# Performance work log

Measured on AMD Instinct MI355X. Metric: run time of the kernel, lower is better.

## Reference

```python
import jax, jax.numpy as jnp
import numpy as np

_S = np.float32(1.0 / np.sqrt(2.0))
_lo = np.array([_S, _S], np.float32)   # dec_lo reversed == rec_lo for db1
_hi = np.array([_S, -_S], np.float32)  # dec_hi reversed == rec_hi for db1
# filters[k][i,j]: k=0 LL/2, k=1 hi(i)*lo(j), k=2 lo(i)*hi(j), k=3 hi*hi  (matches torch unsqueeze outer products)
DEC = np.stack([np.outer(_lo, _lo) / 2.0, np.outer(_hi, _lo), np.outer(_lo, _hi), np.outer(_hi, _hi)]).astype(np.float32)
INV = np.stack([np.outer(_lo, _lo) * 2.0, np.outer(_hi, _lo), np.outer(_lo, _hi), np.outer(_hi, _hi)]).astype(np.float32)
INV_FLIP = np.ascontiguousarray(INV[:, ::-1, ::-1])  # spatially flipped for conv_transpose-as-dilated-conv

DN = ('NCHW', 'OIHW', 'NCHW')


def wt(x):
    # single grouped (depthwise x4) strided conv == per-channel loop in the original
    N, C, H, W = x.shape
    k = jnp.broadcast_to(jnp.asarray(DEC)[None], (C, 4, 2, 2)).reshape(C * 4, 1, 2, 2)
    r = jax.lax.conv_general_dilated(x, k, (2, 2), 'VALID', dimension_numbers=DN, feature_group_count=C)
    r = r.reshape(N, C, 4, H // 2, W // 2)
    r = jnp.concatenate([r[:, :, :1], (r[:, :, 1:] + 1.0) / 2.0], axis=2)  # detail remap
    return r.reshape(N, 4 * C, H // 2, W // 2)


def iwt(v):
    N, C4, H, W = v.shape
    C = C4 // 4
    r = v.reshape(N, C, 4, H, W)
    r = jnp.concatenate([r[:, :, :1], 2.0 * r[:, :, 1:] - 1.0], axis=2).reshape(N, C4, H, W)
    k = jnp.broadcast_to(jnp.asarray(INV_FLIP)[None], (C, 4, 2, 2))
    # conv_transpose2d(stride=2, k=2) == dilated conv with lhs_dilation=2, pad 1, flipped kernel
    return jax.lax.conv_general_dilated(r, k, (1, 1), ((1, 1), (1, 1)), lhs_dilation=(2, 2),
                                        dimension_numbers=DN, feature_group_count=C)


def ws_conv(x, w, b, pad):
    # weight standardization: subtract mean over (in,kh,kw), divide by per-filter std (unbiased) + 1e-5
    wc = w - w.mean(axis=(1, 2, 3), keepdims=True)
    std = wc.reshape(w.shape[0], -1).std(axis=1, ddof=1).reshape(-1, 1, 1, 1) + 1e-5
    y = jax.lax.conv_general_dilated(x, wc / std, (1, 1), ((pad, pad), (pad, pad)), dimension_numbers=DN)
    return y if b is None else y + b[None, :, None, None]


def gn(x, g, b, G):
    N, C, H, W = x.shape
    xr = x.reshape(N, G, -1)
    m = xr.mean(-1, keepdims=True)
    v = xr.var(-1, keepdims=True)
    xr = (xr - m) * jax.lax.rsqrt(v + 1e-5)
    return xr.reshape(N, C, H, W) * g[None, :, None, None] + b[None, :, None, None]


def lrelu(t):
    return jnp.where(t > 0, t, 0.2 * t)


def setup_inputs() -> dict:
    key = jax.random.key(0)
    ks = iter(jax.random.split(key, 32))
    f32 = jnp.float32
    d = {}
    d['x'] = jax.random.normal(next(ks), (16, 3, 256, 256), f32)
    def wgt(shape):
        return 0.05 * jax.random.normal(next(ks), shape, f32)
    def bias(n):
        return 0.01 * jax.random.normal(next(ks), (n,), f32)
    c = 16
    d['conv1_w'], d['conv1_b'] = wgt((c, 12, 3, 3)), bias(c)
    d['conv2_w'], d['conv2_b'] = wgt((4 * c, 4 * c, 3, 3)), bias(4 * c)
    d['conv3_w'], d['conv3_b'] = wgt((16 * c, 16 * c, 3, 3)), bias(16 * c)
    d['conv4_w'], d['conv4_b'] = wgt((64 * c, 64 * c, 3, 3)), bias(64 * c)
    d['convd1_w'], d['convd1_b'] = wgt((12, c, 3, 3)), bias(12)
    d['convd2_w'], d['convd2_b'] = wgt((c, 2 * c, 3, 3)), bias(c)
    d['convd3_w'], d['convd3_b'] = wgt((4 * c, 8 * c, 3, 3)), bias(4 * c)
    d['convd4_w'], d['convd4_b'] = wgt((16 * c, 32 * c, 3, 3)), bias(16 * c)
    d['final_w'] = wgt((2, 3, 1, 1))
    for name, n in (('gn1', c), ('gn2', 4 * c), ('gn3', 16 * c), ('gn4', 64 * c)):
        d[name + '_w'] = 1.0 + 0.1 * jax.random.normal(next(ks), (n,), f32)
        d[name + '_b'] = 0.01 * jax.random.normal(next(ks), (n,), f32)
    return d


def reference(x, conv1_w, conv1_b, conv2_w, conv2_b, conv3_w, conv3_b, conv4_w, conv4_b,
              convd1_w, convd1_b, convd2_w, convd2_b, convd3_w, convd3_b, convd4_w, convd4_b,
              final_w, gn1_w, gn1_b, gn2_w, gn2_b, gn3_w, gn3_b, gn4_w, gn4_b):
    w1 = wt(x)
    c1 = gn(lrelu(ws_conv(w1, conv1_w, conv1_b, 1)), gn1_w, gn1_b, 2)
    w2 = wt(c1)
    c2 = gn(lrelu(ws_conv(w2, conv2_w, conv2_b, 1)), gn2_w, gn2_b, 8)
    w3 = wt(c2)
    c3 = gn(lrelu(ws_conv(w3, conv3_w, conv3_b, 1)), gn3_w, gn3_b, 32)
    w4 = wt(c3)
    c4 = gn(lrelu(ws_conv(w4, conv4_w, conv4_b, 1)), gn4_w, gn4_b, 128)
    c5 = gn(lrelu(ws_conv(c4, conv4_w, conv4_b, 1)), gn4_w, gn4_b, 128)
    c6 = ws_conv(c5, conv4_w, conv4_b, 1)
    ic4 = lrelu(c6 + w4)
    iw4 = jnp.concatenate([c3, iwt(ic4)], axis=1)
    ic3 = gn(lrelu(ws_conv(iw4, convd4_w, convd4_b, 1)), gn3_w, gn3_b, 32)
    iw3 = jnp.concatenate([c2, iwt(ic3)], axis=1)
    ic2 = gn(lrelu(ws_conv(iw3, convd3_w, convd3_b, 1)), gn2_w, gn2_b, 8)
    iw2 = jnp.concatenate([c1, iwt(ic2)], axis=1)
    ic1 = gn(lrelu(ws_conv(iw2, convd2_w, convd2_b, 1)), gn1_w, gn1_b, 2)
    iw1 = lrelu(ws_conv(ic1, convd1_w, convd1_b, 1))
    y = ws_conv(iwt(iw1), final_w, None, 0)
    return y
```

## Files before the change

### kernel.cpp

```cpp
#include <hip/hip_runtime.h>
#include <math.h>


#define NB 16

typedef _Float16 f16;
typedef _Float16 f16x8 __attribute__((ext_vector_type(8)));
typedef _Float16 f16x4 __attribute__((ext_vector_type(4)));
typedef float f32x4 __attribute__((ext_vector_type(4)));
typedef unsigned int u32;

#define LLDS16(gp, lp)                                                          \
  __builtin_amdgcn_global_load_lds((const __attribute__((address_space(1))) u32*)(const void*)(gp), \
                                   (__attribute__((address_space(3))) u32*)(void*)(lp), 16, 0, 0)

__device__ __forceinline__ void ws_reduce(const float* wp, int fan, float* red,
                                          float& mean, float& inv) {
  float s = 0.f, s2 = 0.f;
  for (int i = threadIdx.x; i < fan; i += 256) { float v = wp[i]; s += v; s2 += v * v; }
  red[threadIdx.x] = s; red[256 + threadIdx.x] = s2;
  __syncthreads();
  for (int st = 128; st > 0; st >>= 1) {
    if (threadIdx.x < st) {
      red[threadIdx.x] += red[threadIdx.x + st];
// ... 37 lines not shown
  const float* wp = w + (size_t)oi * fan;
  float mean, inv; ws_reduce(wp, fan, red, mean, inv);
  for (int i = threadIdx.x; i < fan; i += 256) {
    int ci = i / 9, tap = i - ci * 9;
    o[((size_t)tap * Cout + oi) * Cin + ci] = (f16)((wp[i] - mean) * inv);
  }
}

__device__ __forceinline__ void halo_write(f16* buf, int C, int H, int W, int t) {
  int c8s = C >> 3;
  int c8 = t % c8s; int q = t / c8s;
  int P = 2 * (W + 2) + 2 * H;
  int b = q % P; int n = q / P;
  int y, x;
  if (b < W + 2) { y = 0; x = b; }
  else if (b < 2 * (W + 2)) { y = H + 1; x = b - (W + 2); }
  else { int bb = b - 2 * (W + 2); y = 1 + (bb >> 1); x = (bb & 1) ? (W + 1) : 0; }
  size_t a = (((size_t)n * (H + 2) + y) * (W + 2) + x) * C + c8 * 8;
  *(f16x8*)(buf + a) = (f16x8){0, 0, 0, 0, 0, 0, 0, 0};
}

__global__ void halo2_kernel(f16* b0, int c0, int h0, int w0, int n0,
                             f16* b1, int c1, int h1, int w1, int total) {
  int idx = blockIdx.x * 256 + threadIdx.x;
  if (idx >= total) return;
  if (idx < n0) halo_write(b0, c0, h0, w0, idx);
  else halo_write(b1, c1, h1, w1, idx - n0);
}

__global__ void zero_halo_kernel(f16* __restrict__ buf, int C, int H, int W, int total8) {
  int idx = blockIdx.x * 256 + threadIdx.x;
  if (idx >= total8) return;
  halo_write(buf, C, H, W, idx);
}

__global__ void wt_kernel(const float* __restrict__ in, float* __restrict__ out,
                          int C, int Ho, int Wo, int total) {
  int idx = blockIdx.x * 256 + threadIdx.x;
  if (idx >= total) return;
  int w = idx % Wo; int t = idx / Wo;
  int h = t % Ho; t /= Ho;
  int c = t % C; int n = t / C;
  int Wi = 2 * Wo;
  const float* ip = in + (((size_t)n * C + c) * (2 * Ho) + 2 * h) * Wi + 2 * w;
  float a = ip[0], b = ip[1], cc = ip[Wi], d = ip[Wi + 1];
  size_t cs = (size_t)Ho * Wo;
  float* op = out + (((size_t)n * 4 * C + 4 * c) * Ho + h) * Wo + w;
  op[0]      = 0.25f * (a + b + cc + d);
  op[cs]     = 0.25f * (a + b - cc - d) + 0.5f;
  op[2 * cs] = 0.25f * (a - b + cc - d) + 0.5f;
  op[3 * cs] = 0.25f * (a - b - cc + d) + 0.5f;
}

__global__ void iwt_kernel(const float* __restrict__ v, float* __restrict__ out,
                           int C, int H, int W, int c_off, int Ctot, int total) {
  int idx = blockIdx.x * 256 + threadIdx.x;
  if (idx >= total) return;
  int w = idx % W; int t = idx / W;
  int h = t % H; t /= H;
  int c = t % C; int n = t / C;
  size_t cs = (size_t)H * W;
  const float* vp = v + (((size_t)n * 4 * C + 4 * c) * H + h) * W + w;
  float v0 = vp[0];
  float v1 = 2.f * vp[cs] - 1.f;
  float v2 = 2.f * vp[2 * cs] - 1.f;
  float v3 = 2.f * vp[3 * cs] - 1.f;
  int Wo = 2 * W;
  float* op = out + (((size_t)n * Ctot + c_off + c) * (2 * H) + 2 * h) * (size_t)Wo + 2 * w;
  op[0]      = v0 + 0.5f * ( v1 + v2 + v3);
  op[1]      = v0 + 0.5f * ( v1 - v2 - v3);
  op[Wo]     = v0 + 0.5f * (-v1 + v2 - v3);
  op[Wo + 1] = v0 + 0.5f * (-v1 - v2 + v3);
}

__global__ void copycat_kernel(const float* __restrict__ src, float* __restrict__ dst,
                               int C, int HW, int Ctot, int total) {
  int idx = blockIdx.x * 256 + threadIdx.x;
  if (idx >= total) return;
  int p = idx % HW; int t = idx / HW;
  int c = t % C; int n = t / C;
  dst[((size_t)n * Ctot + c) * HW + p] = src[idx];
}

__global__ __launch_bounds__(256) void to_nhwc_pad_kernel(const float* __restrict__ in,
                                                          f16* __restrict__ out,
                                                          int C, int H, int W) {
  __shared__ f16 sm[32][264];
  int HW = H * W;
  int p0 = blockIdx.x * 256, c0 = blockIdx.y * 32, n = blockIdx.z;
  int t = threadIdx.x;
  const float* ip = in + ((size_t)n * C + c0) * HW + p0;
#pragma unroll 8
  for (int r = 0; r < 32; ++r) sm[r][t] = (f16)ip[(size_t)r * HW + t];
  __syncthreads();
#pragma unroll
  for (int i = 0; i < 4; ++i) {
    int c = t + i * 256;
    int pl = c >> 2, cio = (c & 3) * 8;
    f16x8 v;
#pragma unroll
    for (int u = 0; u < 8; ++u) v[u] = sm[cio + u][pl];
    int p = p0 + pl; int y = p / W; int x = p - y * W;
    *(f16x8*)(out + (((size_t)n * (H + 2) + y + 1) * (W + 2) + x + 1) * C + c0 + cio) = v;
  }
}

__global__ __launch_bounds__(256) void gn_nhwc_kernel(
    const float* __restrict__ in, const float* __restrict__ stats,
    const float* __restrict__ gamma, const float* __restrict__ beta,
    f16* __restrict__ out, int C, int H, int W, int G) {
  __shared__ f16 sm[32][264];
  int HW = H * W;
  int p0 = blockIdx.x * 256, c0 = blockIdx.y * 32, n = blockIdx.z;
  int t = threadIdx.x;
  int cpg = C / G;
  const float* ip = in + ((size_t)n * C + c0) * HW + p0;
#pragma unroll 8
  for (int r = 0; r < 32; ++r) {
    int c = c0 + r; int g = c / cpg;
    float mean = stats[(n * G + g) * 2], inv = stats[(n * G + g) * 2 + 1];
    float ga = gamma[c], be = beta[c];
    sm[r][t] = (f16)((ip[(size_t)r * HW + t] - mean) * inv * ga + be);
  }
  __syncthreads();
#pragma unroll
  for (int i = 0; i < 4; ++i) {
    int c = t + i * 256;
    int pl = c >> 2, cio = (c & 3) * 8;
    f16x8 v;
#pragma unroll
    for (int u = 0; u < 8; ++u) v[u] = sm[cio + u][pl];
    int p = p0 + pl; int y = p / W; int x = p - y * W;
    *(f16x8*)(out + (((size_t)n * (H + 2) + y + 1) * (W + 2) + x + 1) * C + c0 + cio) = v;
  }
}

__global__ void iwt_final_kernel(const float* __restrict__ v, const float* __restrict__ w,
                                 float* __restrict__ out, int total) {
  int idx = blockIdx.x * 256 + threadIdx.x;
  if (idx >= total) return;
  int ww = idx % 128; int t = idx / 128;
  int hh = t % 128; int n = t / 128;
  size_t cs = (size_t)128 * 128;
  float y0[3], y1[3], y2[3], y3[3];
#pragma unroll
  for (int c = 0; c < 3; ++c) {
    const float* vp = v + ((size_t)n * 12 + 4 * c) * cs + (size_t)hh * 128 + ww;
    float v0 = vp[0];
    float v1 = 2.f * vp[cs] - 1.f, v2 = 2.f * vp[2 * cs] - 1.f, v3 = 2.f * vp[3 * cs] - 1.f;
    y0[c] = v0 + 0.5f * ( v1 + v2 + v3);
    y1[c] = v0 + 0.5f * ( v1 - v2 - v3);
    y2[c] = v0 + 0.5f * (-v1 + v2 - v3);
    y3[c] = v0 + 0.5f * (-v1 - v2 + v3);
  }
  float w0 = w[0], w1 = w[1], w2 = w[2], w3 = w[3], w4 = w[4], w5 = w[5];
  size_t ocs = (size_t)256 * 256;
  float* o0 = out + (size_t)n * 2 * ocs + (size_t)(2 * hh) * 256 + 2 * ww;
  o0[0]   = w0 * y0[0] + w1 * y0[1] + w2 * y0[2];
  o0[1]   = w0 * y1[0] + w1 * y1[1] + w2 * y1[2];
  o0[256] = w0 * y2[0] + w1 * y2[1] + w2 * y2[2];
  o0[257] = w0 * y3[0] + w1 * y3[1] + w2 * y3[2];
  float* o1 = o0 + ocs;
  o1[0]   = w3 * y0[0] + w4 * y0[1] + w5 * y0[2];
  o1[1]   = w3 * y1[0] + w4 * y1[1] + w5 * y1[2];
  o1[256] = w3 * y2[0] + w4 * y2[1] + w5 * y2[2];
  o1[257] = w3 * y3[0] + w4 * y3[1] + w5 * y3[2];
}

__global__ __launch_bounds__(256) void conv_mfma5_kernel(
    const f16* __restrict__ A, const f16* __restrict__ Wp,
    f16* __restrict__ part, int Cin, int H, int W, int Cout, int HW) {
  constexpr int BM = 128, BN = 128, BK = 64;
  __shared__ f16 Asm[BM * BK];
  __shared__ f16 Bsm[BN * BK];

  const int tid = threadIdx.x;
  const int w = tid >> 6, lane = tid & 63;
  const int m0 = blockIdx.x * BM;
  const int co0 = blockIdx.y * BN;
  const int Wp2 = W + 2;

  const f16* gA[4]; const f16* gB[4];
  int lOff[4];
#pragma unroll
  for (int e = 0; e < 4; ++e) {
    int c = e * 256 + tid;
    int r = c >> 3, j = c & 7;
    int jx = j ^ (r & 7);
    int m = m0 + r; int n = m / HW; int p = m - n * HW;
    int y = p / W; int x = p - y * W;
    gA[e] = A + (((size_t)n * (H + 2) + y + 1) * Wp2 + (x + 1)) * Cin + jx * 8;
    gB[e] = Wp + (size_t)(co0 + r) * Cin + jx * 8;
    lOff[e] = (e * 256 + w * 64) * 8;
  }

  const int wm = w & 1, wn = w >> 1;
  const int lr = lane & 15, quad = lane >> 4;
  int aoffs[4][2], boffs[4][2];
#pragma unroll
  for (int i = 0; i < 4; ++i)
#pragma unroll
    for (int kk = 0; kk < 2; ++kk) {
      int r = wm * 64 + i * 16 + lr;
      int cidx = kk * 4 + quad;
      aoffs[i][kk] = (r * 8 + (cidx ^ (r & 7))) * 8;
      int rb = wn * 64 + i * 16 + lr;
      boffs[i][kk] = (rb * 8 + (cidx ^ (rb & 7))) * 8;
    }

  f32x4 acc[4][4];
#pragma unroll
  for (int i = 0; i < 4; ++i)
#pragma unroll
    for (int j = 0; j < 4; ++j) acc[i][j] = (f32x4){0.f, 0.f, 0.f, 0.f};

  const int kpt = Cin >> 6;
  const int nit = (9 * kpt) / gridDim.z;
  const size_t bstride = (size_t)Cout * Cin;

  int it0 = blockIdx.z * nit;
  int tap = it0 / kpt, kc = (it0 - tap * kpt) << 6;

  for (int ii = 0; ii < nit; ++ii) {
    int dy = tap / 3 - 1, dx = tap % 3 - 1;
    long offA = ((long)dy * Wp2 + dx) * Cin + kc;
    long offB = (long)tap * bstride + kc;
    __syncthreads();
#pragma unroll
    for (int e = 0; e < 4; ++e) {
      LLDS16(gA[e] + offA, Asm + lOff[e]);
      LLDS16(gB[e] + offB, Bsm + lOff[e]);
    }
    __syncthreads();

    f16x8 af[4][2], bf[4][2];
#pragma unroll
    for (int i = 0; i < 4; ++i)
#pragma unroll
      for (int kk = 0; kk < 2; ++kk) {
        af[i][kk] = *(const f16x8*)&Asm[aoffs[i][kk]];
        bf[i][kk] = *(const f16x8*)&Bsm[boffs[i][kk]];
      }
#pragma unroll
    for (int kk = 0; kk < 2; ++kk)
#pragma unroll
      for (int i = 0; i < 4; ++i)
#pragma unroll
        for (int j = 0; j < 4; ++j)
          acc[i][j] = __builtin_amdgcn_mfma_f32_16x16x32_f16(af[i][kk], bf[j][kk], acc[i][j], 0, 0, 0);

    kc += 64;
    if (kc == Cin) { kc = 0; ++tap; }
  }

  const size_t pbase = (size_t)blockIdx.z * NB * Cout * HW;
#pragma unroll
  for (int i = 0; i < 4; ++i) {
    int mg = m0 + wm * 64 + i * 16 + quad * 4;
    int n = mg / HW, p = mg - n * HW;
#pragma unroll
    for (int j = 0; j < 4; ++j) {
      int co = co0 + wn * 64 + j * 16 + lr;
      f32x4 v = acc[i][j];
      f16x4 h;
#pragma unroll
      for (int r = 0; r < 4; ++r) h[r] = (f16)v[r];
      *(f16x4*)&part[pbase + ((size_t)n * Cout + co) * HW + p] = h;
    }
  }
}

__global__ __launch_bounds__(256) void reduceS_kernel(
    const f16* __restrict__ part, const float* __restrict__ bias,
    const float* __restrict__ add, float* __restrict__ out,
    int Cout, int HW, int S, int do_lrelu, int total4) {
  int idx = blockIdx.x * 256 + threadIdx.x;
  if (idx >= total4) return;
  size_t sstride = (size_t)NB * Cout * HW;
  int hw4 = HW >> 2;
  int p4 = idx % hw4; int t = idx / hw4;
  int c = t % Cout;
  size_t eoff = (size_t)t * HW + p4 * 4;
  float b = bias[c];
  f32x4 o = {b, b, b, b};
  for (int s = 0; s < S; ++s) {
    f16x4 a = *(const f16x4*)(part + s * sstride + eoff);
#pragma unroll
    for (int r = 0; r < 4; ++r) o[r] += (float)a[r];
  }
  if (add) {
    f32x4 av = *(const f32x4*)(add + eoff);
#pragma unroll
    for (int r = 0; r < 4; ++r) o[r] += av[r];
  }
  if (do_lrelu)
#pragma unroll
    for (int r = 0; r < 4; ++r) o[r] = o[r] > 0.f ? o[r] : 0.2f * o[r];
  *(f32x4*)(out + eoff) = o;
}

__global__ __launch_bounds__(256) void conv_mfma2_kernel(
    const f16* __restrict__ A, const f16* __restrict__ Wp,
    const float* __restrict__ bias, float* __restrict__ out,
    int Cin, int H, int W, int Cout, int HW, int do_lrelu) {
  constexpr int BM = 128, BN = 64, BK = 64;
  __shared__ f16 Asm[BM * BK];
  __shared__ f16 Bsm[BN * BK];

  const int tid = threadIdx.x;
  const int w = tid >> 6, lane = tid & 63;
  const int m0 = blockIdx.x * BM;
  const int co0 = blockIdx.y * BN;
  const int Wp2 = W + 2;

  const f16* gA[4];
  int lAoff[4];
#pragma unroll
  for (int e = 0; e < 4; ++e) {
    int c = e * 256 + tid;
    int r = c >> 3, j = c & 7;
    int jx = j ^ (r & 7);
    int m = m0 + r; int n = m / HW; int p = m - n * HW;
    int y = p / W; int x = p - y * W;
    gA[e] = A + (((size_t)n * (H + 2) + y + 1) * Wp2 + (x + 1)) * Cin + jx * 8;
    lAoff[e] = (e * 256 + w * 64) * 8;
  }
  const f16* gB[2];
  int lBoff[2];
#pragma unroll
  for (int e = 0; e < 2; ++e) {
    int c = e * 256 + tid;
    int r = c >> 3, j = c & 7;
    int jx = j ^ (r & 7);
    gB[e] = Wp + (size_t)(co0 + r) * Cin + jx * 8;
    lBoff[e] = (e * 256 + w * 64) * 8;
  }

  const int wm = w & 1, wn = w >> 1;
  const int lr = lane & 15, quad = lane >> 4;
  int aoffs[4][2], boffs[2][2];
#pragma unroll
  for (int i = 0; i < 4; ++i)
#pragma unroll
    for (int kk = 0; kk < 2; ++kk) {
      int r = wm * 64 + i * 16 + lr;
      int cidx = kk * 4 + quad;
      aoffs[i][kk] = (r * 8 + (cidx ^ (r & 7))) * 8;
    }
#pragma unroll
  for (int jn = 0; jn < 2; ++jn)
#pragma unroll
// ... 13 lines not shown
    const int dy = tap / 3 - 1, dx = tap % 3 - 1;
    const long tapA = ((long)dy * Wp2 + dx) * Cin;
    const long tapB = (size_t)tap * Cout * Cin;
    for (int kc = 0; kc < Cin; kc += BK) {
      __syncthreads();
#pragma unroll
      for (int e = 0; e < 4; ++e) LLDS16(gA[e] + tapA + kc, Asm + lAoff[e]);
#pragma unroll
      for (int e = 0; e < 2; ++e) LLDS16(gB[e] + tapB + kc, Bsm + lBoff[e]);
      __syncthreads();

      f16x8 af[4][2], bf[2][2];
#pragma unroll
      for (int i = 0; i < 4; ++i)
#pragma unroll
        for (int kk = 0; kk < 2; ++kk) af[i][kk] = *(const f16x8*)&Asm[aoffs[i][kk]];
#pragma unroll
      for (int jn = 0; jn < 2; ++jn)
#pragma unroll
        for (int kk = 0; kk < 2; ++kk) bf[jn][kk] = *(const f16x8*)&Bsm[boffs[jn][kk]];
#pragma unroll
      for (int kk = 0; kk < 2; ++kk)
#pragma unroll
        for (int i = 0; i < 4; ++i)
#pragma unroll
          for (int jn = 0; jn < 2; ++jn)
            acc[i][jn] = __builtin_amdgcn_mfma_f32_16x16x32_f16(af[i][kk], bf[jn][kk], acc[i][jn], 0, 0, 0);
    }
  }

#pragma unroll
  for (int i = 0; i < 4; ++i) {
    int mg = m0 + wm * 64 + i * 16 + quad * 4;
    int n = mg / HW, p = mg - n * HW;
#pragma unroll
    for (int jn = 0; jn < 2; ++jn) {
      int co = co0 + wn * 32 + jn * 16 + lr;
      float b = bias[co];
      f32x4 v = acc[i][jn];
#pragma unroll
      for (int r = 0; r < 4; ++r) {
        float u = v[r] + b;
        v[r] = (do_lrelu && u < 0.f) ? 0.2f * u : u;
      }
      *(f32x4*)&out[((size_t)n * Cout + co) * HW + p] = v;
    }
  }
}

template <int CO, int CIC>
__global__ __launch_bounds__(256) void conv3x3_kernel(
    const float* __restrict__ in, const float* __restrict__ wgt,
    const float* __restrict__ bias, float* __restrict__ out,
    int Cin, int H, int W, int Cout, int do_lrelu) {
  __shared__ float sm[CIC][18][18];
  int tiles_x = W >> 4;
  int bt = blockIdx.x;
  int tx0 = (bt % tiles_x) << 4;
  int ty0 = (bt / tiles_x) << 4;
  int co0 = blockIdx.y * CO;
  int n = blockIdx.z;
  int tid = threadIdx.x;
  int lx = tid & 15, ly = tid >> 4;

  float acc[CO];
#pragma unroll
  for (int i = 0; i < CO; i++) acc[i] = 0.f;

  const float* inb = in + (size_t)n * Cin * H * W;

  for (int ci0 = 0; ci0 < Cin; ci0 += CIC) {
    __syncthreads();
    for (int idx = tid; idx < CIC * 324; idx += 256) {
      int ci = idx / 324;
      int r = idx - ci * 324;
      int gy = r / 18, gx = r - gy * 18;
      int iy = ty0 + gy - 1, ix = tx0 + gx - 1;
      float v = 0.f;
      if ((unsigned)iy < (unsigned)H && (unsigned)ix < (unsigned)W)
        v = inb[((size_t)(ci0 + ci)) * H * W + (size_t)iy * W + ix];
      sm[ci][gy][gx] = v;
    }
    __syncthreads();
#pragma unroll
    for (int ci = 0; ci < CIC; ci++) {
      float x00 = sm[ci][ly][lx],     x01 = sm[ci][ly][lx + 1],     x02 = sm[ci][ly][lx + 2];
      float x10 = sm[ci][ly + 1][lx], x11 = sm[ci][ly + 1][lx + 1], x12 = sm[ci][ly + 1][lx + 2];
      float x20 = sm[ci][ly + 2][lx], x21 = sm[ci][ly + 2][lx + 1], x22 = sm[ci][ly + 2][lx + 2];
      const float* wp = wgt + ((size_t)co0 * Cin + (ci0 + ci)) * 9;
#pragma unroll
      for (int co = 0; co < CO; co++) {
        const float* wc = wp + (size_t)co * Cin * 9;
        float a = acc[co];
        a = fmaf(wc[0], x00, a); a = fmaf(wc[1], x01, a); a = fmaf(wc[2], x02, a);
        a = fmaf(wc[3], x10, a); a = fmaf(wc[4], x11, a); a = fmaf(wc[5], x12, a);
        a = fmaf(wc[6], x20, a); a = fmaf(wc[7], x21, a); a = fmaf(wc[8], x22, a);
        acc[co] = a;
      }
    }
  }

  int oy = ty0 + ly, ox = tx0 + lx;
#pragma unroll
  for (int co = 0; co < CO; co++) {
    float v = acc[co] + bias[co0 + co];
    if (do_lrelu) v = v > 0.f ? v : 0.2f * v;
    out[(((size_t)n * Cout + co0 + co) * H + oy) * W + ox] = v;
  }
}

__global__ __launch_bounds__(256) void gn_stats_kernel(const float* __restrict__ x,
                                                       float* __restrict__ part,
                                                       int C, int HW, int G, int SPLIT) {
  __shared__ float red[512];
  int gs = blockIdx.x;
  int g = gs / SPLIT, s = gs - g * SPLIT;
  int n = blockIdx.y;
  int cpg = C / G;
  int len = cpg * HW;
  int chunk = len / SPLIT;
  size_t base = ((size_t)n * C + (size_t)g * cpg) * HW + (size_t)s * chunk;
  const f32x4* xp = (const f32x4*)(x + base);
  int chunk4 = chunk >> 2;
  float sm = 0.f, s2 = 0.f;
  for (int i = threadIdx.x; i < chunk4; i += 256) {
    f32x4 v = xp[i];
    sm += v.x + v.y + v.z + v.w;
    s2 += v.x * v.x + v.y * v.y + v.z * v.z + v.w * v.w;
  }
  red[threadIdx.x] = sm; red[256 + threadIdx.x] = s2;
  __syncthreads();
  for (int st = 128; st > 0; st >>= 1) {
    if (threadIdx.x < st) {
      red[threadIdx.x] += red[threadIdx.x + st];
      red[256 + threadIdx.x] += red[256 + threadIdx.x + st];
    }
    __syncthreads();
  }
  if (threadIdx.x == 0) {
    int o = ((n * G + g) * SPLIT + s) * 2;
    part[o] = red[0]; part[o + 1] = red[256];
  }
}

__global__ void gn_combine_kernel(const float* __restrict__ part, float* __restrict__ stats,
                                  int SPLIT, int len, int total) {
  int idx = blockIdx.x * 256 + threadIdx.x;
  if (idx >= total) return;
  float s = 0.f, s2 = 0.f;
  for (int i = 0; i < SPLIT; ++i) { s += part[(idx * SPLIT + i) * 2]; s2 += part[(idx * SPLIT + i) * 2 + 1]; }
  float mean = s / (float)len;
  float var = s2 / (float)len - mean * mean;
  if (var < 0.f) var = 0.f;
  stats[idx * 2] = mean;
  stats[idx * 2 + 1] = rsqrtf(var + 1e-5f);
}

__global__ __launch_bounds__(256) void gn_apply_kernel(float* __restrict__ x,
                                                       const float* __restrict__ stats,
                                                       const float* __restrict__ gamma,
                                                       const float* __restrict__ beta,
                                                       int C, int HW, int G, int total4) {
  int idx = blockIdx.x * 256 + threadIdx.x;
  if (idx >= total4) return;
  int hw4 = HW >> 2;
  int p4 = idx % hw4; int t = idx / hw4;
  int c = t % C; int n = t / C;
  int cpg = C / G; int g = c / cpg;
  float mean = stats[(n * G + g) * 2];
  float inv  = stats[(n * G + g) * 2 + 1];
  float ga = gamma[c], be = beta[c];
  f32x4* xp = (f32x4*)(x + ((size_t)t * HW)) + p4;
  f32x4 v = *xp;
#pragma unroll
  for (int r = 0; r < 4; ++r) v[r] = (v[r] - mean) * inv * ga + be;
  *xp = v;
}


extern "C" void kernel_launch(void* const* d_in, const int* in_sizes, int n_in,
                              void* d_out, int out_size, void* d_ws, size_t ws_size,
                              hipStream_t stream) {
  const float* x        = (const float*)d_in[0];
  const float* conv1_w  = (const float*)d_in[1];
  const float* conv1_b  = (const float*)d_in[2];
  const float* conv2_w  = (const float*)d_in[3];
  const float* conv2_b  = (const float*)d_in[4];
  const float* conv3_w  = (const float*)d_in[5];
  const float* conv3_b  = (const float*)d_in[6];
  const float* conv4_w  = (const float*)d_in[7];
  const float* conv4_b  = (const float*)d_in[8];
  const float* convd1_w = (const float*)d_in[9];
  const float* convd1_b = (const float*)d_in[10];
  const float* convd2_w = (const float*)d_in[11];
  const float* convd2_b = (const float*)d_in[12];
  const float* convd3_w = (const float*)d_in[13];
  const float* convd3_b = (const float*)d_in[14];
  const float* convd4_w = (const float*)d_in[15];
  const float* convd4_b = (const float*)d_in[16];
  const float* final_w  = (const float*)d_in[17];
  const float* gn1_w = (const float*)d_in[18];
  const float* gn1_b = (const float*)d_in[19];
  const float* gn2_w = (const float*)d_in[20];
  const float* gn2_b = (const float*)d_in[21];
  const float* gn3_w = (const float*)d_in[22];
  const float* gn3_b = (const float*)d_in[23];
  const float* gn4_w = (const float*)d_in[24];
  const float* gn4_b = (const float*)d_in[25];

  char* base = (char*)d_ws;
  size_t off = 0;
  auto allocB = [&](size_t bytes) { size_t o = off; off = (off + bytes + 255) & ~(size_t)255; return o; };

  size_t o_sw1  = allocB(16 * 108 * 4);
  size_t o_swd1 = allocB(12 * 144 * 4);
  size_t o_swd2 = allocB(16 * 288 * 4);
  size_t o_swf  = allocB(6 * 4);
  size_t o_pw2  = allocB((size_t)9 * 64 * 64 * 2);
  size_t o_pw3  = allocB((size_t)9 * 256 * 256 * 2);
  size_t o_pw4  = allocB((size_t)9 * 1024 * 1024 * 2);
  size_t o_pwd3 = allocB((size_t)9 * 64 * 128 * 2);
  size_t o_pwd4 = allocB((size_t)9 * 256 * 512 * 2);
  size_t o_R1   = allocB((size_t)NB * 66 * 66 * 128 * 2);
  size_t o_R2   = allocB((size_t)NB * 34 * 34 * 512 * 2);
  size_t o_gnp  = allocB(4096 * 4);
  size_t o_gns  = allocB(4096 * 4);
  size_t o_c1 = allocB((size_t)NB * 16 * 128 * 128 * 4);
  size_t o_c2 = allocB((size_t)NB * 64 * 64 * 64 * 4);
  size_t o_c3 = allocB((size_t)NB * 256 * 32 * 32 * 4);
  size_t o_w4 = allocB((size_t)NB * 1024 * 16 * 16 * 4);
  size_t o_t1 = allocB((size_t)NB * 1024 * 16 * 16 * 4);
  size_t o_t2 = allocB((size_t)NB * 512 * 32 * 32 * 4);

  if (off > ws_size) return;

  float* c1 = (float*)(base + o_c1);
  float* c2 = (float*)(base + o_c2);
  float* c3 = (float*)(base + o_c3);
  float* w4 = (float*)(base + o_w4);
  float* t1 = (float*)(base + o_t1);
  float* t2 = (float*)(base + o_t2);
  f16* part  = (f16*)(base + o_R1);
  f16* ah64  = (f16*)(base + o_R1);
  f16* ah128 = (f16*)(base + o_R1);
  f16* ah256 = (f16*)(base + o_R2);
  f16* ah1k  = (f16*)(base + o_R2);
  f16* ah512 = (f16*)(base + o_R2);
  f16* pw2 = (f16*)(base + o_pw2);
  f16* pw3 = (f16*)(base + o_pw3);
  f16* pw4 = (f16*)(base + o_pw4);
  f16* pwd3 = (f16*)(base + o_pwd3);
  f16* pwd4 = (f16*)(base + o_pwd4);
  float* gnp = (float*)(base + o_gnp);
  float* gns = (float*)(base + o_gns);

  {
    int n0 = NB * (2 * 66 + 2 * 64) * (64 / 8);
    int n1 = NB * (2 * 34 + 2 * 32) * (256 / 8);
    int tot = n0 + n1;
    halo2_kernel<<<(tot + 255) / 256, 256, 0, stream>>>(ah64, 64, 64, 64, n0,
                                                        ah256, 256, 32, 32, tot);
  }
  ws_all_kernel<<<46, 256, 0, stream>>>(conv1_w, (float*)(base + o_sw1),
                                        convd1_w, (float*)(base + o_swd1),
                                        convd2_w, (float*)(base + o_swd2),
                                        final_w, (float*)(base + o_swf));
  ws_f16_all_kernel<<<1664, 256, 0, stream>>>(conv2_w, pw2, conv3_w, pw3, conv4_w, pw4,
                                              convd3_w, pwd3, convd4_w, pwd4);

  auto gn_sc = [&](const float* xb, int C, int HW, int G) {
    int SPLIT = 2048 / (G * NB);
    if (SPLIT < 1) SPLIT = 1;
    int len = (C / G) * HW;
    dim3 gsd(G * SPLIT, NB);
    gn_stats_kernel<<<gsd, 256, 0, stream>>>(xb, gnp, C, HW, G, SPLIT);
    int tot = NB * G;
    gn_combine_kernel<<<(tot + 255) / 256, 256, 0, stream>>>(gnp, gns, SPLIT, len, tot);
  };
  auto gn_full = [&](float* xb, const float* g, const float* b, int C, int HW, int G) {
    gn_sc(xb, C, HW, G);
    int total4 = (NB * C * HW) >> 2;
    gn_apply_kernel<<<(total4 + 255) / 256, 256, 0, stream>>>(xb, gns, g, b, C, HW, G, total4);
  };
  auto prep_nhwc = [&](const float* in, f16* ah, int C, int H, int W, int zero) {
    if (zero) {
      int total8 = NB * (2 * (W + 2) + 2 * H) * (C / 8);
      zero_halo_kernel<<<(total8 + 255) / 256, 256, 0, stream>>>(ah, C, H, W, total8);
    }
    dim3 g((H * W) / 256, C / 32, NB);
    to_nhwc_pad_kernel<<<g, 256, 0, stream>>>(in, ah, C, H, W);
  };
  auto cm5 = [&](const f16* a, const f16* wt, const float* b, float* dest, const float* add,
                 int Cin, int Hs, int Ws, int Cout, int lr) {
    dim3 g((NB * Hs * Ws) / 128, Cout / 128, 2);
    conv_mfma5_kernel<<<g, 256, 0, stream>>>(a, wt, part, Cin, Hs, Ws, Cout, Hs * Ws);
    int total4 = (NB * Cout * Hs * Ws) >> 2;
    reduceS_kernel<<<(total4 + 255) / 256, 256, 0, stream>>>(part, b, add, dest,
                                                             Cout, Hs * Ws, 2, lr, total4);
  };
  auto cm2 = [&](const f16* a, const f16* wt, const float* b, float* o,
                 int Cin, int Hs, int Ws, int Cout, int lr) {
    dim3 g((NB * Hs * Ws) / 128, Cout / 64);
    conv_mfma2_kernel<<<g, 256, 0, stream>>>(a, wt, b, o, Cin, Hs, Ws, Cout, Hs * Ws, lr);
  };
  auto launch_wt = [&](const float* in, float* out, int C, int Ho, int Wo) {
    int total = NB * C * Ho * Wo;
    wt_kernel<<<(total + 255) / 256, 256, 0, stream>>>(in, out, C, Ho, Wo, total);
  };
  auto launch_iwt = [&](const float* v, float* out, int C, int H, int W, int c_off, int Ctot) {
    int total = NB * C * H * W;
    iwt_kernel<<<(total + 255) / 256, 256, 0, stream>>>(v, out, C, H, W, c_off, Ctot, total);
  };
  auto launch_copycat = [&](const float* src, float* dst, int C, int HW, int Ctot) {
    int total = NB * C * HW;
    copycat_kernel<<<(total + 255) / 256, 256, 0, stream>>>(src, dst, C, HW, Ctot, total);
  };

  launch_wt(x, t1, 3, 128, 128);
  {
    dim3 g(64, 1, NB);
    conv3x3_kernel<16, 4><<<g, 256, 0, stream>>>(t1, (float*)(base + o_sw1), conv1_b,
                                                 c1, 12, 128, 128, 16, 1);
  }
  gn_full(c1, gn1_w, gn1_b, 16, 128 * 128, 2);

  launch_wt(c1, t1, 16, 64, 64);
  prep_nhwc(t1, ah64, 64, 64, 64, 0);
  cm2(ah64, pw2, conv2_b, c2, 64, 64, 64, 64, 1);
  gn_full(c2, gn2_w, gn2_b, 64, 64 * 64, 8);

  launch_wt(c2, t1, 64, 32, 32);
  prep_nhwc(t1, ah256, 256, 32, 32, 0);
  cm5(ah256, pw3, conv3_b, c3, nullptr, 256, 32, 32, 256, 1);
  gn_full(c3, gn3_w, gn3_b, 256, 32 * 32, 32);

  launch_wt(c3, w4, 256, 16, 16);
  prep_nhwc(w4, ah1k, 1024, 16, 16, 1);

  cm5(ah1k, pw4, conv4_b, t1, nullptr, 1024, 16, 16, 1024, 1);
  gn_sc(t1, 1024, 256, 128);
  {
    dim3 g(1, 32, NB);
    gn_nhwc_kernel<<<g, 256, 0, stream>>>(t1, gns, gn4_w, gn4_b, ah1k, 1024, 16, 16, 128);
  }
  cm5(ah1k, pw4, conv4_b, t2, nullptr, 1024, 16, 16, 1024, 1);
  gn_sc(t2, 1024, 256, 128);
  {
    dim3 g(1, 32, NB);
    gn_nhwc_kernel<<<g, 256, 0, stream>>>(t2, gns, gn4_w, gn4_b, ah1k, 1024, 16, 16, 128);
  }
  cm5(ah1k, pw4, conv4_b, t1, w4, 1024, 16, 16, 1024, 1);

  launch_copycat(c3, t2, 256, 32 * 32, 512);
  launch_iwt(t1, t2, 256, 16, 16, 256, 512);
  prep_nhwc(t2, ah512, 512, 32, 32, 1);
  cm5(ah512, pwd4, convd4_b, t1, nullptr, 512, 32, 32, 256, 1);
  gn_full(t1, gn3_w, gn3_b, 256, 32 * 32, 32);

  launch_copycat(c2, t2, 64, 64 * 64, 128);
  launch_iwt(t1, t2, 64, 32, 32, 64, 128);
  prep_nhwc(t2, ah128, 128, 64, 64, 1);
  cm2(ah128, pwd3, convd3_b, t1, 128, 64, 64, 64, 1);
  gn_full(t1, gn2_w, gn2_b, 64, 64 * 64, 8);

  launch_copycat(c1, t2, 16, 128 * 128, 32);
  launch_iwt(t1, t2, 16, 64, 64, 16, 32);
  {
    dim3 g(64, 1, NB);
    conv3x3_kernel<16, 4><<<g, 256, 0, stream>>>(t2, (float*)(base + o_swd2), convd2_b,
                                                 t1, 32, 128, 128, 16, 1);
  }
  gn_full(t1, gn1_w, gn1_b, 16, 128 * 128, 2);
  {
    dim3 g(64, 1, NB);
    conv3x3_kernel<12, 4><<<g, 256, 0, stream>>>(t1, (float*)(base + o_swd1), convd1_b,
                                                 t2, 16, 128, 128, 12, 1);
  }
  {
    int total = NB * 128 * 128;
    iwt_final_kernel<<<(total + 255) / 256, 256, 0, stream>>>(t2, (float*)(base + o_swf),
                                                              (float*)d_out, total);
  }
}
```

Measured before the change: 1.025 ms.

## Fuse GroupNorm stats into conv epilogues, merge concat+iwt, double-buffer MFMA conv

```diff
diff --git a/kernel.cpp b/kernel.cpp
--- a/kernel.cpp
+++ b/kernel.cpp
@@ -113,34 +113,46 @@
   op[3 * cs] = 0.25f * (a - b - cc + d) + 0.5f;
 }
 
-__global__ void iwt_kernel(const float* __restrict__ v, float* __restrict__ out,
-                           int C, int H, int W, int c_off, int Ctot, int total) {
+__global__ void concat_iwt_kernel(const float* __restrict__ skip, const float* __restrict__ v,
+                                  float* __restrict__ out, const float* __restrict__ gnp,
+                                  const float* __restrict__ gamma, const float* __restrict__ beta,
+                                  int G, int Sg, int len, int C, int Hh, int Wh,
+                                  int totalA, int total) {
   int idx = blockIdx.x * 256 + threadIdx.x;
   if (idx >= total) return;
-  int w = idx % W; int t = idx / W;
-  int h = t % H; t /= H;
+  int W = 2 * Wh, H = 2 * Hh; int HWs = H * W;
+  if (idx < totalA) {
+    int p = idx % HWs; int t = idx / HWs; int c = t % C; int n = t / C;
+    out[((size_t)n * 2 * C + c) * HWs + p] = skip[idx];
+    return;
+  }
+  int i2 = idx - totalA;
+  int w = i2 % Wh; int t = i2 / Wh; int h = t % Hh; t /= Hh;
   int c = t % C; int n = t / C;
-  size_t cs = (size_t)H * W;
-  const float* vp = v + (((size_t)n * 4 * C + 4 * c) * H + h) * W + w;
-  float v0 = vp[0];
-  float v1 = 2.f * vp[cs] - 1.f;
-  float v2 = 2.f * vp[2 * cs] - 1.f;
-  float v3 = 2.f * vp[3 * cs] - 1.f;
-  int Wo = 2 * W;
-  float* op = out + (((size_t)n * Ctot + c_off + c) * (2 * H) + 2 * h) * (size_t)Wo + 2 * w;
-  op[0]      = v0 + 0.5f * ( v1 + v2 + v3);
-  op[1]      = v0 + 0.5f * ( v1 - v2 - v3);
-  op[Wo]     = v0 + 0.5f * (-v1 + v2 - v3);
-  op[Wo + 1] = v0 + 0.5f * (-v1 - v2 + v3);
-}
-
-__global__ void copycat_kernel(const float* __restrict__ src, float* __restrict__ dst,
-                               int C, int HW, int Ctot, int total) {
-  int idx = blockIdx.x * 256 + threadIdx.x;
-  if (idx >= total) return;
-  int p = idx % HW; int t = idx / HW;
-  int c = t % C; int n = t / C;
-  dst[((size_t)n * Ctot + c) * HW + p] = src[idx];
+  size_t cs = (size_t)Hh * Wh;
+  const float* vp = v + (((size_t)n * 4 * C + 4 * c) * Hh + h) * Wh + w;
+  float v0 = vp[0], v1 = vp[cs], v2 = vp[2 * cs], v3 = vp[3 * cs];
+  if (gnp) {
+    int cpg = (4 * C) / G;
+    int g = (4 * c) / cpg;
+    const float* pp = gnp + (size_t)((n * G + g) * Sg) * 2;
+    float s = 0.f, s2 = 0.f;
+    for (int i = 0; i < Sg; ++i) { s += pp[2 * i]; s2 += pp[2 * i + 1]; }
+    float mean = s / (float)len;
+    float var = s2 / (float)len - mean * mean;
+    if (var < 0.f) var = 0.f;
+    float inv = rsqrtf(var + 1e-5f);
+    v0 = (v0 - mean) * inv * gamma[4 * c]     + beta[4 * c];
+    v1 = (v1 - mean) * inv * gamma[4 * c + 1] + beta[4 * c + 1];
+    v2 = (v2 - mean) * inv * gamma[4 * c + 2] + beta[4 * c + 2];
+    v3 = (v3 - mean) * inv * gamma[4 * c + 3] + beta[4 * c + 3];
+  }
+  v1 = 2.f * v1 - 1.f; v2 = 2.f * v2 - 1.f; v3 = 2.f * v3 - 1.f;
+  float* op = out + (((size_t)n * 2 * C + C + c) * H + 2 * h) * (size_t)W + 2 * w;
+  op[0]     = v0 + 0.5f * ( v1 + v2 + v3);
+  op[1]     = v0 + 0.5f * ( v1 - v2 - v3);
+  op[W]     = v0 + 0.5f * (-v1 + v2 - v3);
+  op[W + 1] = v0 + 0.5f * (-v1 - v2 + v3);
 }
 
 __global__ __launch_bounds__(256) void to_nhwc_pad_kernel(const float* __restrict__ in,
@@ -167,9 +179,9 @@
 }
 
 __global__ __launch_bounds__(256) void gn_nhwc_kernel(
-    const float* __restrict__ in, const float* __restrict__ stats,
+    const float* __restrict__ in, const float* __restrict__ gnp,
     const float* __restrict__ gamma, const float* __restrict__ beta,
-    f16* __restrict__ out, int C, int H, int W, int G) {
+    f16* __restrict__ out, int C, int H, int W, int G, int Sg, int len) {
   __shared__ f16 sm[32][264];
   int HW = H * W;
   int p0 = blockIdx.x * 256, c0 = blockIdx.y * 32, n = blockIdx.z;
@@ -179,7 +191,13 @@
 #pragma unroll 8
   for (int r = 0; r < 32; ++r) {
     int c = c0 + r; int g = c / cpg;
-    float mean = stats[(n * G + g) * 2], inv = stats[(n * G + g) * 2 + 1];
+    const float* pp = gnp + (size_t)((n * G + g) * Sg) * 2;
+    float s = 0.f, s2 = 0.f;
+    for (int i = 0; i < Sg; ++i) { s += pp[2 * i]; s2 += pp[2 * i + 1]; }
+    float mean = s / (float)len;
+    float var = s2 / (float)len - mean * mean;
+    if (var < 0.f) var = 0.f;
+    float inv = rsqrtf(var + 1e-5f);
     float ga = gamma[c], be = beta[c];
     sm[r][t] = (f16)((ip[(size_t)r * HW + t] - mean) * inv * ga + be);
   }
@@ -228,17 +246,17 @@
   o1[257] = w3 * y3[0] + w4 * y3[1] + w5 * y3[2];
 }
 
-__global__ __launch_bounds__(256) void conv_mfma5_kernel(
+__global__ __launch_bounds__(256) void conv_mfma6_kernel(
     const f16* __restrict__ A, const f16* __restrict__ Wp,
     f16* __restrict__ part, int Cin, int H, int W, int Cout, int HW) {
-  constexpr int BM = 128, BN = 128, BK = 64;
-  __shared__ f16 Asm[BM * BK];
-  __shared__ f16 Bsm[BN * BK];
+  constexpr int CH = 128 * 64;
+  __shared__ f16 Asm[2 * CH];
+  __shared__ f16 Bsm[2 * CH];
 
   const int tid = threadIdx.x;
   const int w = tid >> 6, lane = tid & 63;
-  const int m0 = blockIdx.x * BM;
-  const int co0 = blockIdx.y * BN;
+  const int m0 = blockIdx.x * 128;
+  const int co0 = blockIdx.y * 128;
   const int Wp2 = W + 2;
 
   const f16* gA[4]; const f16* gB[4];
@@ -277,30 +295,37 @@
 
   const int kpt = Cin >> 6;
   const int nit = (9 * kpt) / gridDim.z;
+  const int it0 = blockIdx.z * nit;
   const size_t bstride = (size_t)Cout * Cin;
 
-  int it0 = blockIdx.z * nit;
-  int tap = it0 / kpt, kc = (it0 - tap * kpt) << 6;
-
+  auto stageAB = [&](int it, int sel) {
+    int tap = it / kpt, kk = it - tap * kpt;
+    int dy = tap / 3 - 1, dx = tap % 3 - 1;
+    long offA = ((long)dy * Wp2 + dx) * Cin + (kk << 6);
+    long offB = (long)tap * bstride + (kk << 6);
+    f16* ab = Asm + sel * CH;
+    f16* bb = Bsm + sel * CH;
+#pragma unroll
+    for (int e = 0; e < 4; ++e) {
+      LLDS16(gA[e] + offA, ab + lOff[e]);
+      LLDS16(gB[e] + offB, bb + lOff[e]);
+    }
+  };
+
+  stageAB(it0, 0);
+  int sel = 0;
   for (int ii = 0; ii < nit; ++ii) {
-    int dy = tap / 3 - 1, dx = tap % 3 - 1;
-    long offA = ((long)dy * Wp2 + dx) * Cin + kc;
-    long offB = (long)tap * bstride + kc;
     __syncthreads();
-#pragma unroll
-    for (int e = 0; e < 4; ++e) {
-      LLDS16(gA[e] + offA, Asm + lOff[e]);
-      LLDS16(gB[e] + offB, Bsm + lOff[e]);
-    }
-    __syncthreads();
-
+    if (ii + 1 < nit) stageAB(it0 + ii + 1, sel ^ 1);
+    const f16* ab = Asm + sel * CH;
+    const f16* bb = Bsm + sel * CH;
     f16x8 af[4][2], bf[4][2];
 #pragma unroll
     for (int i = 0; i < 4; ++i)
 #pragma unroll
       for (int kk = 0; kk < 2; ++kk) {
-        af[i][kk] = *(const f16x8*)&Asm[aoffs[i][kk]];
-        bf[i][kk] = *(const f16x8*)&Bsm[boffs[i][kk]];
+        af[i][kk] = *(const f16x8*)&ab[aoffs[i][kk]];
+        bf[i][kk] = *(const f16x8*)&bb[boffs[i][kk]];
       }
 #pragma unroll
     for (int kk = 0; kk < 2; ++kk)
@@ -309,9 +334,7 @@
 #pragma unroll
         for (int j = 0; j < 4; ++j)
           acc[i][j] = __builtin_amdgcn_mfma_f32_16x16x32_f16(af[i][kk], bf[j][kk], acc[i][j], 0, 0, 0);
-
-    kc += 64;
-    if (kc == Cin) { kc = 0; ++tap; }
+    sel ^= 1;
   }
 
   const size_t pbase = (size_t)blockIdx.z * NB * Cout * HW;
@@ -334,7 +357,9 @@
 __global__ __launch_bounds__(256) void reduceS_kernel(
     const f16* __restrict__ part, const float* __restrict__ bias,
     const float* __restrict__ add, float* __restrict__ out,
-    int Cout, int HW, int S, int do_lrelu, int total4) {
+    int Cout, int HW, int S, int do_lrelu, int total4,
+    float* __restrict__ gnp, int G, int Sg) {
+  __shared__ float red[512];
   int idx = blockIdx.x * 256 + threadIdx.x;
   if (idx >= total4) return;
   size_t sstride = (size_t)NB * Cout * HW;
@@ -358,6 +383,30 @@
 #pragma unroll
     for (int r = 0; r < 4; ++r) o[r] = o[r] > 0.f ? o[r] : 0.2f * o[r];
   *(f32x4*)(out + eoff) = o;
+  if (gnp) {
+    float ls = o[0] + o[1] + o[2] + o[3];
+    float ls2 = o[0]*o[0] + o[1]*o[1] + o[2]*o[2] + o[3]*o[3];
+    red[threadIdx.x] = ls; red[256 + threadIdx.x] = ls2;
+    __syncthreads();
+    for (int st = 128; st > 0; st >>= 1) {
+      if (threadIdx.x < st) {
+        red[threadIdx.x] += red[threadIdx.x + st];
+        red[256 + threadIdx.x] += red[256 + threadIdx.x + st];
+      }
+      __syncthreads();
+    }
+    if (threadIdx.x == 0) {
+      int flat0 = blockIdx.x * 1024;
+      int chw = Cout * HW;
+      int n = flat0 / chw;
+      int rem = flat0 - n * chw;
+      int L = (Cout / G) * HW;
+      int g = rem / L;
+      int s = (rem - g * L) >> 10;
+      gnp[((n * G + g) * Sg + s) * 2] = red[0];
+      gnp[((n * G + g) * Sg + s) * 2 + 1] = red[256];
+    }
+  }
 }
 
 __global__ __launch_bounds__(256) void conv_mfma2_kernel(
@@ -477,7 +526,7 @@
 __global__ __launch_bounds__(256) void conv3x3_kernel(
     const float* __restrict__ in, const float* __restrict__ wgt,
     const float* __restrict__ bias, float* __restrict__ out,
-    int Cin, int H, int W, int Cout, int do_lrelu) {
+    int Cin, int H, int W, int Cout, int do_lrelu, float* __restrict__ gnp) {
   __shared__ float sm[CIC][18][18];
   int tiles_x = W >> 4;
   int bt = blockIdx.x;
@@ -525,13 +574,44 @@
     }
   }
 
-  int oy = ty0 + ly, ox = tx0 + lx;
+  float vout[CO];
 #pragma unroll
   for (int co = 0; co < CO; co++) {
     float v = acc[co] + bias[co0 + co];
     if (do_lrelu) v = v > 0.f ? v : 0.2f * v;
-    out[(((size_t)n * Cout + co0 + co) * H + oy) * W + ox] = v;
-  }
+    vout[co] = v;
+  }
+
+  if (gnp) {
+    float p0 = 0.f, q0 = 0.f, p1 = 0.f, q1 = 0.f;
+#pragma unroll
+    for (int co = 0; co < 8; ++co) { p0 += vout[co]; q0 += vout[co] * vout[co]; }
+#pragma unroll
+    for (int co = 8; co < CO; ++co) { p1 += vout[co]; q1 += vout[co] * vout[co]; }
+    float* red = &sm[0][0][0];
+    __syncthreads();
+    red[tid] = p0; red[256 + tid] = q0; red[512 + tid] = p1; red[768 + tid] = q1;
+    __syncthreads();
+    for (int st = 128; st > 0; st >>= 1) {
+      if (tid < st) {
+        red[tid] += red[tid + st]; red[256 + tid] += red[256 + tid + st];
+        red[512 + tid] += red[512 + tid + st]; red[768 + tid] += red[768 + tid + st];
+      }
+      __syncthreads();
+    }
+    if (tid == 0) {
+      int S = gridDim.x;
+      gnp[((n * 2 + 0) * S + blockIdx.x) * 2]     = red[0];
+      gnp[((n * 2 + 0) * S + blockIdx.x) * 2 + 1] = red[256];
+      gnp[((n * 2 + 1) * S + blockIdx.x) * 2]     = red[512];
+      gnp[((n * 2 + 1) * S + blockIdx.x) * 2 + 1] = red[768];
+    }
+  }
+
+  int oy = ty0 + ly, ox = tx0 + lx;
+#pragma unroll
+  for (int co = 0; co < CO; co++)
+    out[(((size_t)n * Cout + co0 + co) * H + oy) * W + ox] = vout[co];
 }
 
 __global__ __launch_bounds__(256) void gn_stats_kernel(const float* __restrict__ x,
@@ -568,32 +648,30 @@
   }
 }
 
-__global__ void gn_combine_kernel(const float* __restrict__ part, float* __restrict__ stats,
-                                  int SPLIT, int len, int total) {
+__global__ __launch_bounds__(256) void gn_apply_kernel(float* __restrict__ x,
+                                                       const float* __restrict__ gnp,
+                                                       const float* __restrict__ gamma,
+                                                       const float* __restrict__ beta,
+                                                       int C, int HW, int G, int Sg, int len,
+                                                       int total4) {
   int idx = blockIdx.x * 256 + threadIdx.x;
-  if (idx >= total) return;
+  if (idx >= total4) return;
+  int flat0 = blockIdx.x * 1024;
+  int chw = C * HW;
+  int n = flat0 / chw;
+  int rem = flat0 - n * chw;
+  int L = (C / G) * HW;
+  int g = rem / L;
+  const float* pp = gnp + (size_t)((n * G + g) * Sg) * 2;
   float s = 0.f, s2 = 0.f;
-  for (int i = 0; i < SPLIT; ++i) { s += part[(idx * SPLIT + i) * 2]; s2 += part[(idx * SPLIT + i) * 2 + 1]; }
+  for (int i = 0; i < Sg; ++i) { s += pp[2 * i]; s2 += pp[2 * i + 1]; }
   float mean = s / (float)len;
   float var = s2 / (float)len - mean * mean;
   if (var < 0.f) var = 0.f;
-  stats[idx * 2] = mean;
-  stats[idx * 2 + 1] = rsqrtf(var + 1e-5f);
-}
-
-__global__ __launch_bounds__(256) void gn_apply_kernel(float* __restrict__ x,
-                                                       const float* __restrict__ stats,
-                                                       const float* __restrict__ gamma,
-                                                       const float* __restrict__ beta,
-                                                       int C, int HW, int G, int total4) {
-  int idx = blockIdx.x * 256 + threadIdx.x;
-  if (idx >= total4) return;
+  float inv = rsqrtf(var + 1e-5f);
   int hw4 = HW >> 2;
   int p4 = idx % hw4; int t = idx / hw4;
-  int c = t % C; int n = t / C;
-  int cpg = C / G; int g = c / cpg;
-  float mean = stats[(n * G + g) * 2];
-  float inv  = stats[(n * G + g) * 2 + 1];
+  int c = t % C;
   float ga = gamma[c], be = beta[c];
   f32x4* xp = (f32x4*)(x + ((size_t)t * HW)) + p4;
   f32x4 v = *xp;
@@ -648,8 +726,7 @@
   size_t o_pwd4 = allocB((size_t)9 * 256 * 512 * 2);
   size_t o_R1   = allocB((size_t)NB * 66 * 66 * 128 * 2);
   size_t o_R2   = allocB((size_t)NB * 34 * 34 * 512 * 2);
-  size_t o_gnp  = allocB(4096 * 4);
-  size_t o_gns  = allocB(4096 * 4);
+  size_t o_gnp  = allocB(16384 * 4);
   size_t o_c1 = allocB((size_t)NB * 16 * 128 * 128 * 4);
   size_t o_c2 = allocB((size_t)NB * 64 * 64 * 64 * 4);
   size_t o_c3 = allocB((size_t)NB * 256 * 32 * 32 * 4);
@@ -677,7 +754,6 @@
   f16* pwd3 = (f16*)(base + o_pwd3);
   f16* pwd4 = (f16*)(base + o_pwd4);
   float* gnp = (float*)(base + o_gnp);
-  float* gns = (float*)(base + o_gns);
 
   {
     int n0 = NB * (2 * 66 + 2 * 64) * (64 / 8);
@@ -693,20 +769,6 @@
   ws_f16_all_kernel<<<1664, 256, 0, stream>>>(conv2_w, pw2, conv3_w, pw3, conv4_w, pw4,
                                               convd3_w, pwd3, convd4_w, pwd4);
 
-  auto gn_sc = [&](const float* xb, int C, int HW, int G) {
-    int SPLIT = 2048 / (G * NB);
-    if (SPLIT < 1) SPLIT = 1;
-    int len = (C / G) * HW;
-    dim3 gsd(G * SPLIT, NB);
-    gn_stats_kernel<<<gsd, 256, 0, stream>>>(xb, gnp, C, HW, G, SPLIT);
-    int tot = NB * G;
-    gn_combine_kernel<<<(tot + 255) / 256, 256, 0, stream>>>(gnp, gns, SPLIT, len, tot);
-  };
-  auto gn_full = [&](float* xb, const float* g, const float* b, int C, int HW, int G) {
-    gn_sc(xb, C, HW, G);
-    int total4 = (NB * C * HW) >> 2;
-    gn_apply_kernel<<<(total4 + 255) / 256, 256, 0, stream>>>(xb, gns, g, b, C, HW, G, total4);
-  };
   auto prep_nhwc = [&](const float* in, f16* ah, int C, int H, int W, int zero) {
     if (zero) {
       int total8 = NB * (2 * (W + 2) + 2 * H) * (C / 8);
@@ -715,13 +777,13 @@
     dim3 g((H * W) / 256, C / 32, NB);
     to_nhwc_pad_kernel<<<g, 256, 0, stream>>>(in, ah, C, H, W);
   };
-  auto cm5 = [&](const f16* a, const f16* wt, const float* b, float* dest, const float* add,
-                 int Cin, int Hs, int Ws, int Cout, int lr) {
+  auto cm6 = [&](const f16* a, const f16* wt, const float* b, float* dest, const float* add,
+                 int Cin, int Hs, int Ws, int Cout, int lr, int G, int Sg) {
     dim3 g((NB * Hs * Ws) / 128, Cout / 128, 2);
-    conv_mfma5_kernel<<<g, 256, 0, stream>>>(a, wt, part, Cin, Hs, Ws, Cout, Hs * Ws);
+    conv_mfma6_kernel<<<g, 256, 0, stream>>>(a, wt, part, Cin, Hs, Ws, Cout, Hs * Ws);
     int total4 = (NB * Cout * Hs * Ws) >> 2;
-    reduceS_kernel<<<(total4 + 255) / 256, 256, 0, stream>>>(part, b, add, dest,
-                                                             Cout, Hs * Ws, 2, lr, total4);
+    reduceS_kernel<<<(total4 + 255) / 256, 256, 0, stream>>>(
+        part, b, add, dest, Cout, Hs * Ws, 2, lr, total4, G ? gnp : nullptr, G, Sg);
   };
   auto cm2 = [&](const f16* a, const f16* wt, const float* b, float* o,
                  int Cin, int Hs, int Ws, int Cout, int lr) {
@@ -732,74 +794,79 @@
     int total = NB * C * Ho * Wo;
     wt_kernel<<<(total + 255) / 256, 256, 0, stream>>>(in, out, C, Ho, Wo, total);
   };
-  auto launch_iwt = [&](const float* v, float* out, int C, int H, int W, int c_off, int Ctot) {
-    int total = NB * C * H * W;
-    iwt_kernel<<<(total + 255) / 256, 256, 0, stream>>>(v, out, C, H, W, c_off, Ctot, total);
+  auto apply = [&](float* xb, const float* g, const float* b, int C, int HW, int G, int Sg) {
+    int len = (C / G) * HW;
+    int total4 = (NB * C * HW) >> 2;
+    gn_apply_kernel<<<(total4 + 255) / 256, 256, 0, stream>>>(xb, gnp, g, b, C, HW, G, Sg,
+                                                              len, total4);
   };
-  auto launch_copycat = [&](const float* src, float* dst, int C, int HW, int Ctot) {
-    int total = NB * C * HW;
-    copycat_kernel<<<(total + 255) / 256, 256, 0, stream>>>(src, dst, C, HW, Ctot, total);
+  auto stats = [&](const float* xb, int C, int HW, int G, int SPLIT) {
+    dim3 gsd(G * SPLIT, NB);
+    gn_stats_kernel<<<gsd, 256, 0, stream>>>(xb, gnp, C, HW, G, SPLIT);
+  };
+  auto concat_iwt = [&](const float* skip, const float* v, float* out, int C, int Hh, int Wh,
+                        const float* gg, const float* gb, int G, int Sg) {
+    int totalA = NB * C * 4 * Hh * Wh;
+    int total = totalA + NB * C * Hh * Wh;
+    int len = G ? ((4 * C) / G) * Hh * Wh : 1;
+    concat_iwt_kernel<<<(total + 255) / 256, 256, 0, stream>>>(
+        skip, v, out, G ? gnp : nullptr, gg, gb, G, Sg, len, C, Hh, Wh, totalA, total);
   };
 
   launch_wt(x, t1, 3, 128, 128);
   {
     dim3 g(64, 1, NB);
     conv3x3_kernel<16, 4><<<g, 256, 0, stream>>>(t1, (float*)(base + o_sw1), conv1_b,
-                                                 c1, 12, 128, 128, 16, 1);
-  }
-  gn_full(c1, gn1_w, gn1_b, 16, 128 * 128, 2);
+                                                 c1, 12, 128, 128, 16, 1, gnp);
+  }
+  apply(c1, gn1_w, gn1_b, 16, 128 * 128, 2, 64);
 
   launch_wt(c1, t1, 16, 64, 64);
   prep_nhwc(t1, ah64, 64, 64, 64, 0);
   cm2(ah64, pw2, conv2_b, c2, 64, 64, 64, 64, 1);
-  gn_full(c2, gn2_w, gn2_b, 64, 64 * 64, 8);
+  stats(c2, 64, 4096, 8, 16);
+  apply(c2, gn2_w, gn2_b, 64, 4096, 8, 16);
 
   launch_wt(c2, t1, 64, 32, 32);
   prep_nhwc(t1, ah256, 256, 32, 32, 0);
-  cm5(ah256, pw3, conv3_b, c3, nullptr, 256, 32, 32, 256, 1);
-  gn_full(c3, gn3_w, gn3_b, 256, 32 * 32, 32);
+  cm6(ah256, pw3, conv3_b, c3, nullptr, 256, 32, 32, 256, 1, 32, 8);
+  apply(c3, gn3_w, gn3_b, 256, 1024, 32, 8);
 
   launch_wt(c3, w4, 256, 16, 16);
   prep_nhwc(w4, ah1k, 1024, 16, 16, 1);
 
-  cm5(ah1k, pw4, conv4_b, t1, nullptr, 1024, 16, 16, 1024, 1);
-  gn_sc(t1, 1024, 256, 128);
+  cm6(ah1k, pw4, conv4_b, t1, nullptr, 1024, 16, 16, 1024, 1, 128, 2);
   {
     dim3 g(1, 32, NB);
-    gn_nhwc_kernel<<<g, 256, 0, stream>>>(t1, gns, gn4_w, gn4_b, ah1k, 1024, 16, 16, 128);
-  }
-  cm5(ah1k, pw4, conv4_b, t2, nullptr, 1024, 16, 16, 1024, 1);
-  gn_sc(t2, 1024, 256, 128);
+    gn_nhwc_kernel<<<g, 256, 0, stream>>>(t1, gnp, gn4_w, gn4_b, ah1k, 1024, 16, 16,
+                                          128, 2, 2048);
+  }
+  cm6(ah1k, pw4, conv4_b, t2, nullptr, 1024, 16, 16, 1024, 1, 128, 2);
   {
     dim3 g(1, 32, NB);
-    gn_nhwc_kernel<<<g, 256, 0, stream>>>(t2, gns, gn4_w, gn4_b, ah1k, 1024, 16, 16, 128);
-  }
-  cm5(ah1k, pw4, conv4_b, t1, w4, 1024, 16, 16, 1024, 1);
-
-  launch_copycat(c3, t2, 256, 32 * 32, 512);
-  launch_iwt(t1, t2, 256, 16, 16, 256, 512);
+    gn_nhwc_kernel<<<g, 256, 0, stream>>>(t2, gnp, gn4_w, gn4_b, ah1k, 1024, 16, 16,
+                                          128, 2, 2048);
+  }
+  cm6(ah1k, pw4, conv4_b, t1, w4, 1024, 16, 16, 1024, 1, 0, 0);
+
+  concat_iwt(c3, t1, t2, 256, 16, 16, nullptr, nullptr, 0, 0);
   prep_nhwc(t2, ah512, 512, 32, 32, 1);
-  cm5(ah512, pwd4, convd4_b, t1, nullptr, 512, 32, 32, 256, 1);
-  gn_full(t1, gn3_w, gn3_b, 256, 32 * 32, 32);
-
-  launch_copycat(c2, t2, 64, 64 * 64, 128);
-  launch_iwt(t1, t2, 64, 32, 32, 64, 128);
+  cm6(ah512, pwd4, convd4_b, t1, nullptr, 512, 32, 32, 256, 1, 32, 8);
+  concat_iwt(c2, t1, t2, 64, 32, 32, gn3_w, gn3_b, 32, 8);
   prep_nhwc(t2, ah128, 128, 64, 64, 1);
   cm2(ah128, pwd3, convd3_b, t1, 128, 64, 64, 64, 1);
-  gn_full(t1, gn2_w, gn2_b, 64, 64 * 64, 8);
-
-  launch_copycat(c1, t2, 16, 128 * 128, 32);
-  launch_iwt(t1, t2, 16, 64, 64, 16, 32);
+  stats(t1, 64, 4096, 8, 16);
+  concat_iwt(c1, t1, t2, 16, 64, 64, gn2_w, gn2_b, 8, 16);
   {
     dim3 g(64, 1, NB);
     conv3x3_kernel<16, 4><<<g, 256, 0, stream>>>(t2, (float*)(base + o_swd2), convd2_b,
-                                                 t1, 32, 128, 128, 16, 1);
-  }
-  gn_full(t1, gn1_w, gn1_b, 16, 128 * 128, 2);
+                                                 t1, 32, 128, 128, 16, 1, gnp);
+  }
+  apply(t1, gn1_w, gn1_b, 16, 128 * 128, 2, 64);
   {
     dim3 g(64, 1, NB);
     conv3x3_kernel<12, 4><<<g, 256, 0, stream>>>(t1, (float*)(base + o_swd1), convd1_b,
-                                                 t2, 16, 128, 128, 12, 1);
+                                                 t2, 16, 128, 128, 12, 1, nullptr);
   }
   {
     int total = NB * 128 * 128;
```

Result: faster. 943.0 us (-8.0%).
